# Kernel optimization log

Hardware: AMD Instinct MI355X
Metric: run time of the kernel (lower is better)

Reference implementation:

```python
import jax, jax.numpy as jnp
import numpy as np

N, E, D_IN, D_OUT, MAX_DEG = 50000, 800000, 128, 128, 64
ALPHA = 0.5


def _linear_params(key, fan_in, fan_out):
    s = 1.0 / np.sqrt(fan_in)
    kw, kb = jax.random.split(key)
    W = jax.random.uniform(kw, (fan_out, fan_in), jnp.float32, -s, s)
    b = jax.random.uniform(kb, (fan_out,), jnp.float32, -s, s)
    return W, b


def setup_inputs() -> dict:
    key = jax.random.key(0)
    ks = jax.random.split(key, 16)
    x = jax.random.normal(ks[0], (N, D_IN), jnp.float32)
    edge_index = jax.random.randint(ks[1], (2, E), 0, N, dtype=jnp.int64)
    in_degree = jax.random.randint(ks[2], (N,), 0, MAX_DEG, dtype=jnp.int64)
    out_degree = jax.random.randint(ks[3], (N,), 0, MAX_DEG, dtype=jnp.int64)
    out_deg_mask = jax.random.uniform(ks[4], (N,), jnp.float32)
    out_deg_mask_bias = jax.random.uniform(ks[5], (N,), jnp.float32)
    in_deg_mask = jax.random.uniform(ks[6], (N,), jnp.float32)
    in_deg_mask_bias = jax.random.uniform(ks[7], (N,), jnp.float32)
    W_src, b_src = _linear_params(ks[8], D_IN, D_OUT)
    W_dst, b_dst = _linear_params(ks[9], D_IN, D_OUT)
    W_out_f, b_out_f = _linear_params(ks[10], D_IN, 1)
    W_in_f, b_in_f = _linear_params(ks[11], D_IN, 1)
    W_fc, b_fc = _linear_params(ks[12], D_IN, D_OUT)
    # degree embedding tables, padding_idx=0 -> row 0 zeroed
    in_deg_table = (jax.random.normal(ks[13], (MAX_DEG, D_IN), jnp.float32)).at[0].set(0.0)
    out_deg_table = (jax.random.normal(ks[14], (MAX_DEG, D_IN), jnp.float32)).at[0].set(0.0)
    return {
        "x": x, "edge_index": edge_index,
        "in_degree": in_degree, "out_degree": out_degree,
        "out_deg_mask": out_deg_mask, "out_deg_mask_bias": out_deg_mask_bias,
        "in_deg_mask": in_deg_mask, "in_deg_mask_bias": in_deg_mask_bias,
        "W_src": W_src, "b_src": b_src, "W_dst": W_dst, "b_dst": b_dst,
        "W_out_f": W_out_f, "b_out_f": b_out_f, "W_in_f": W_in_f, "b_in_f": b_in_f,
        "W_fc": W_fc, "b_fc": b_fc,
        "in_deg_table": in_deg_table, "out_deg_table": out_deg_table,
    }


def reference(x, edge_index, in_degree, out_degree,
              out_deg_mask, out_deg_mask_bias, in_deg_mask, in_deg_mask_bias,
              W_src, b_src, W_dst, b_dst,
              W_out_f, b_out_f, W_in_f, b_in_f,
              W_fc, b_fc, in_deg_table, out_deg_table):
    n = x.shape[0]
    row, col = edge_index[0], edge_index[1]
    ones = jnp.ones(row.shape[0], x.dtype)
    # directed norm D_out^{-1/2} A D_in^{-1/2}; transpose reuses the same edge weights
    out_deg = jax.ops.segment_sum(ones, row, num_segments=n)
    in_deg = jax.ops.segment_sum(ones, col, num_segments=n)
    o_inv = jnp.where(out_deg > 0, jax.lax.rsqrt(jnp.maximum(out_deg, 1e-12)), 0.0)
    i_inv = jnp.where(in_deg > 0, jax.lax.rsqrt(jnp.maximum(in_deg, 1e-12)), 0.0)
    w = o_inv[row] * i_inv[col]  # [E]
    # adj_norm @ x and adj_t_norm @ x (SpMM via gather + segment_sum)
    out_nei = jax.ops.segment_sum(w[:, None] * x[col], row, num_segments=n)  # [N,D]
    in_nei = jax.ops.segment_sum(w[:, None] * x[row], col, num_segments=n)   # [N,D]
    # degree-gated filter
    c_out = (out_nei - x + out_deg_table[out_degree]) @ W_out_f.T + b_out_f  # [N,1]
    c_in = (in_nei - x + in_deg_table[in_degree]) @ W_in_f.T + b_in_f        # [N,1]
    C = jax.nn.softmax(jnp.concatenate([c_out, c_in], axis=1), axis=1)        # tau_softmax, tau=1
    C_out = C[:, 0:1] * out_deg_mask[:, None] + out_deg_mask_bias[:, None]
    C_in = C[:, 1:2] * in_deg_mask[:, None] + in_deg_mask_bias[:, None]
    out = (C_out * (out_nei @ W_src.T + b_src)
           + C_in * (in_nei @ W_dst.T + b_dst)
           + ALPHA * (x @ W_fc.T + b_fc))
    return out, C_in, C_out
```

## Files before the change

kernel.cpp:

```cpp
#include <hip/hip_runtime.h>

#define NN 50000
#define EE 800000
#define DD 128
#define CAP 48
#define MT 64
#define XSL 6250
#define PB 128

typedef short short8_t __attribute__((ext_vector_type(8)));
typedef float f32x4 __attribute__((ext_vector_type(4)));

__device__ __forceinline__ unsigned short f2bf(float f) {
    union { float f; unsigned int i; } v; v.f = f;
    unsigned int x = v.i;
    x += 0x7FFFu + ((x >> 16) & 1u);
    return (unsigned short)(x >> 16);
}
__device__ __forceinline__ unsigned int pack2(float a, float b) {
    return (unsigned int)f2bf(a) | ((unsigned int)f2bf(b) << 16);
}
__device__ __forceinline__ float2 bf2x2(unsigned int u) {
    union { unsigned int i; float f; } lo, hi;
    lo.i = u << 16;
    hi.i = u & 0xFFFF0000u;
    return make_float2(lo.f, hi.f);
}

__device__ __forceinline__ void acc8(float4& a, float4& b, uint4 u, float w) {
    float2 p0 = bf2x2(u.x), p1 = bf2x2(u.y), p2 = bf2x2(u.z), p3 = bf2x2(u.w);
    a.x += w * p0.x; a.y += w * p0.y; a.z += w * p1.x; a.w += w * p1.y;
    b.x += w * p2.x; b.y += w * p2.y; b.z += w * p3.x; b.w += w * p3.y;
}

__global__ void k_conv(const float* __restrict__ x,
                       const float* __restrict__ W_src,
                       const float* __restrict__ W_dst,
                       const float* __restrict__ W_fc,
                       unsigned short* __restrict__ xb,
                       unsigned short* __restrict__ wbf) {
    int t = blockIdx.x * 256 + threadIdx.x;
    int base = t * 4;
    if (base < NN * DD) {
        float4 v = *(const float4*)(x + base);
        uint2 p; p.x = pack2(v.x, v.y); p.y = pack2(v.z, v.w);
        *(uint2*)(xb + base) = p;
    } else {
        int b2 = base - NN * DD;
        if (b2 < 3 * 16384) {
            int src = b2 >> 14;
            int off = b2 & 16383;
            const float* W = (src == 0) ? W_src : (src == 1) ? W_dst : W_fc;
            float sc = (src == 2) ? 0.5f : 1.0f;
            float4 v = *(const float4*)(W + off);
            uint2 p; p.x = pack2(v.x * sc, v.y * sc); p.y = pack2(v.z * sc, v.w * sc);
            *(uint2*)(wbf + b2) = p;
        }
    }
}

__global__ void __launch_bounds__(256) k_place(
    const int* __restrict__ ei, int* __restrict__ cnt,
    unsigned short* __restrict__ bkt_row, unsigned short* __restrict__ bkt_col) {
    int xcd = blockIdx.x & 7;
    int b   = blockIdx.x >> 3;
    int lo = xcd * XSL, hi = lo + XSL;
    for (int e = b * 256 + threadIdx.x; e < EE; e += PB * 256) {
        int r = ei[e];
        int c = ei[EE + e];
        if (r >= lo && r < hi) {
            int po = atomicAdd(&cnt[r], 1);
            if (po < CAP) bkt_row[(size_t)r * CAP + po] = (unsigned short)c;
        }
        if (c >= lo && c < hi) {
            int pi = atomicAdd(&cnt[NN + c], 1);
            if (pi < CAP) bkt_col[(size_t)c * CAP + pi] = (unsigned short)r;
        }
    }
}

__global__ void __launch_bounds__(256) k_prep(
    const int* __restrict__ cnt, const float4* __restrict__ x4,
    float* __restrict__ invb, float* __restrict__ w2, uint2* __restrict__ xs2)
{
    int t = blockIdx.x * 256 + threadIdx.x;
    if (t < 2 * NN) {
        int d = cnt[t];
        invb[t] = (d > 0) ? (1.0f / sqrtf((float)d)) : 0.0f;
    }
    if (t < NN) {
        int dd = cnt[t];
        int di = cnt[NN + t];
        float o = (dd > 0) ? (1.0f / sqrtf((float)dd)) : 0.0f;
        w2[t] = (di > 0) ? o * sqrtf((float)di) : o;
    }
    if (t < NN * 32) {
        int node = t >> 5;
        int di = cnt[NN + node];
        float s = (di > 0) ? (1.0f / sqrtf((float)di)) : 1.0f;
        float4 v = x4[t];
        uint2 p; p.x = pack2(v.x * s, v.y * s); p.y = pack2(v.z * s, v.w * s);
        xs2[t] = p;
    }
}

__global__ void __launch_bounds__(256) k_gather(
    const uint4* __restrict__ xs4, const float4* __restrict__ x4,
    const unsigned short* __restrict__ bkt_row, const unsigned short* __restrict__ bkt_col,
    const int* __restrict__ cnt,
    const float* __restrict__ o_inv, const float* __restrict__ i_inv,
    const float* __restrict__ w2,
    const int* __restrict__ in_degree, const int* __restrict__ out_degree,
    const float* __restrict__ odm, const float* __restrict__ odmb,
    const float* __restrict__ idm, const float* __restrict__ idmb,
    const float4* __restrict__ W_out_f4, const float* __restrict__ b_out_f,
    const float4* __restrict__ W_in_f4, const float* __restrict__ b_in_f,
    const float4* __restrict__ in_tab4, const float4* __restrict__ out_tab4,
    uint2* __restrict__ onb2, uint2* __restrict__ inb2,
    float* __restrict__ scbuf,
    float* __restrict__ outCin, float* __restrict__ outCout)
{
    __shared__ float4 sred[2][4][2][16][2];
    __shared__ float sg[2][2];
    __shared__ float sC[2][2];
    int half = threadIdx.x >> 7;
    int n = blockIdx.x * 2 + half;
    int t = threadIdx.x & 127;
    int g = t >> 5;
    int l = t & 31;
    int dir = g >> 1;
    int gd  = g & 1;
    int sub = l >> 4;
    int li  = l & 15;
    int shamt = gd << 4;

    const unsigned short* bp = ((dir == 0) ? bkt_row : bkt_col) + (size_t)n * CAP;
    int deg = cnt[dir * NN + n]; deg = (deg > CAP) ? CAP : deg;

    unsigned int bw = (l < 24) ? *(const unsigned int*)(bp + 2 * l) : 0u;

    float w_l = 0.0f;
    if (dir == 1) {
        unsigned int pr = __shfl(bw, l >> 1, 32);
        int il = (pr >> ((l & 1) << 4)) & 0xffff;
        if (l < deg) w_l = w2[il];
    }

    float4 ac0 = make_float4(0.f, 0.f, 0.f, 0.f);
    float4 ac1 = make_float4(0.f, 0.f, 0.f, 0.f);

    if (dir == 0 || deg <= 32) {
        int j = gd;
        for (; j + 14 < deg; j += 16) {
            int s0 = j + 2 * sub, s1 = s0 + 4, s2 = s0 + 8, s3 = s0 + 12;
            int i0 = (__shfl(bw, s0 >> 1, 32) >> shamt) & 0xffff;
            int i1 = (__shfl(bw, s1 >> 1, 32) >> shamt) & 0xffff;
            int i2 = (__shfl(bw, s2 >> 1, 32) >> shamt) & 0xffff;
            int i3 = (__shfl(bw, s3 >> 1, 32) >> shamt) & 0xffff;
            uint4 u0 = xs4[(size_t)i0 * 16 + li];
            uint4 u1 = xs4[(size_t)i1 * 16 + li];
            uint4 u2 = xs4[(size_t)i2 * 16 + li];
            uint4 u3 = xs4[(size_t)i3 * 16 + li];
            float w0 = 1.f, w1 = 1.f, w2v = 1.f, w3 = 1.f;
            if (dir) {
                w0  = __shfl(w_l, s0, 32);
                w1  = __shfl(w_l, s1, 32);
                w2v = __shfl(w_l, s2, 32);
                w3  = __shfl(w_l, s3, 32);
            }
            acc8(ac0, ac1, u0, w0);
            acc8(ac0, ac1, u1, w1);
            acc8(ac0, ac1, u2, w2v);
            acc8(ac0, ac1, u3, w3);
        }
        for (; j + 6 < deg; j += 8) {
            int s0 = j + 2 * sub, s1 = s0 + 4;
            int i0 = (__shfl(bw, s0 >> 1, 32) >> shamt) & 0xffff;
            int i1 = (__shfl(bw, s1 >> 1, 32) >> shamt) & 0xffff;
            uint4 u0 = xs4[(size_t)i0 * 16 + li];
            uint4 u1 = xs4[(size_t)i1 * 16 + li];
            float w0 = 1.f, w1 = 1.f;
            if (dir) {
                w0 = __shfl(w_l, s0, 32);
                w1 = __shfl(w_l, s1, 32);
            }
            acc8(ac0, ac1, u0, w0);
            acc8(ac0, ac1, u1, w1);
        }
        for (; j < deg; j += 4) {
            int s0 = j + 2 * sub;
            int sc = (s0 < deg) ? s0 : gd;
            int i0 = (__shfl(bw, sc >> 1, 32) >> shamt) & 0xffff;
            float w0 = 1.f;
            if (dir) w0 = __shfl(w_l, sc, 32);
            if (s0 < deg) {
                uint4 u0 = xs4[(size_t)i0 * 16 + li];
                acc8(ac0, ac1, u0, w0);
            }
        }
    } else {
        for (int j = gd; j < deg; j += 4) {
            int s0 = j + 2 * sub;
            int sc = (s0 < deg) ? s0 : gd;
            int i0 = (__shfl(bw, sc >> 1, 32) >> shamt) & 0xffff;
            if (s0 < deg) {
                float w0 = w2[i0];
                uint4 u0 = xs4[(size_t)i0 * 16 + li];
                acc8(ac0, ac1, u0, w0);
            }
        }
    }

    sred[half][g][sub][li][0] = ac0;
    sred[half][g][sub][li][1] = ac1;
    __syncthreads();

    float4 r = make_float4(0.f, 0.f, 0.f, 0.f);
    if (gd == 0) {
        int src = l >> 1, q = l & 1;
        int g0 = dir * 2;
        float4 b0 = sred[half][g0][0][src][q];
        float4 b1 = sred[half][g0][1][src][q];
        float4 b2 = sred[half][g0 + 1][0][src][q];
        float4 b3 = sred[half][g0 + 1][1][src][q];
        float wn = (dir == 0) ? o_inv[n] : i_inv[n];
        r.x = wn * (b0.x + b1.x + b2.x + b3.x);
        r.y = wn * (b0.y + b1.y + b2.y + b3.y);
        r.z = wn * (b0.z + b1.z + b2.z + b3.z);
        r.w = wn * (b0.w + b1.w + b2.w + b3.w);
        float4 xv = x4[(size_t)n * 32 + l];
        float4 tb, wf;
        if (dir == 0) {
            int odg = out_degree[n];
            odg = (odg < 0) ? 0 : (odg > 63 ? 63 : odg);
            tb = out_tab4[(size_t)odg * 32 + l];
            wf = W_out_f4[l];
        } else {
            int idg = in_degree[n];
            idg = (idg < 0) ? 0 : (idg > 63 ? 63 : idg);
            tb = in_tab4[(size_t)idg * 32 + l];
            wf = W_in_f4[l];
        }
        float p = (r.x - xv.x + tb.x) * wf.x + (r.y - xv.y + tb.y) * wf.y
                + (r.z - xv.z + tb.z) * wf.z + (r.w - xv.w + tb.w) * wf.w;
        #pragma unroll
        for (int off = 16; off > 0; off >>= 1) p += __shfl_down(p, off);
        if (l == 0) sg[half][dir] = p;
    }
    __syncthreads();
    if (t == 0) {
        float c_out = sg[half][0] + b_out_f[0];
        float c_in  = sg[half][1] + b_in_f[0];
        float m  = fmaxf(c_out, c_in);
        float eo = expf(c_out - m);
        float e2 = expf(c_in  - m);
        float inv = 1.0f / (eo + e2);
        float Cout = (eo * inv) * odm[n] + odmb[n];
        float Cin  = (e2 * inv) * idm[n] + idmb[n];
        sC[half][0] = Cout; sC[half][1] = Cin;
        scbuf[2 * n]     = Cout;
        scbuf[2 * n + 1] = Cin;
        outCout[n] = Cout;
        outCin[n]  = Cin;
    }
    __syncthreads();
    if (gd == 0) {
        float C = sC[half][dir];
        uint2 pw; pw.x = pack2(C * r.x, C * r.y); pw.y = pack2(C * r.z, C * r.w);
        ((dir == 0) ? onb2 : inb2)[(size_t)n * 32 + l] = pw;
    }
}

__global__ void __launch_bounds__(256) k_gemm(
    const unsigned int* __restrict__ xb32,
    const unsigned int* __restrict__ onb32, const unsigned int* __restrict__ inb32,
    const unsigned short* __restrict__ wbf,
    const float* __restrict__ b_src, const float* __restrict__ b_dst,
    const float* __restrict__ b_fc,
    const float* __restrict__ scbuf,
    float* __restrict__ out)
{
    __shared__ unsigned short sA[MT * 72];
    __shared__ unsigned short sBt[DD * 72];

    int tid = threadIdx.x;
    int wid = tid >> 6;
    int lane = tid & 63;
    int ml = lane & 15;
    int kq = lane >> 4;
    int n0 = blockIdx.x * MT;

    f32x4 accv[8];
    #pragma unroll
    for (int i = 0; i < 8; i++) accv[i] = (f32x4)0.0f;

    const unsigned int* srcs[3] = { onb32, inb32, xb32 };

    for (int kt = 0; kt < 6; kt++) {
        int srcsel = kt >> 1;
        int k0 = (kt & 1) * 64;
        const unsigned int* S = srcs[srcsel];

        #pragma unroll
        for (int r = 0; r < 2; r++) {
            int s = tid + 256 * r;
            int row = s >> 3;
            int cg = s & 7;
            int gn = n0 + row;
            uint4 p = make_uint4(0u, 0u, 0u, 0u);
            if (gn < NN) {
                p = *(const uint4*)(S + (size_t)gn * 64 + (k0 >> 1) + cg * 4);
            }
            *(uint4*)(sA + row * 72 + cg * 8) = p;
        }
        #pragma unroll
        for (int r = 0; r < 4; r++) {
            int s = tid + 256 * r;
            int row = s >> 3;
            int cg = s & 7;
            uint4 w = *(const uint4*)(wbf + srcsel * 16384 + row * DD + k0 + cg * 8);
            *(uint4*)(sBt + row * 72 + cg * 8) = w;
        }
        __syncthreads();

        #pragma unroll
        for (int ks = 0; ks < 64; ks += 32) {
            short8_t a = *(const short8_t*)(sA + (16 * wid + ml) * 72 + ks + kq * 8);
            #pragma unroll
            for (int i = 0; i < 8; i++) {
                short8_t b = *(const short8_t*)(sBt + (16 * i + ml) * 72 + ks + kq * 8);
                accv[i] = __builtin_amdgcn_mfma_f32_16x16x32_bf16(a, b, accv[i], 0, 0, 0);
            }
        }
        __syncthreads();
    }

    int row_base = n0 + 16 * wid + 4 * kq;
    #pragma unroll
    for (int r = 0; r < 4; r++) {
        int row = row_base + r;
        if (row >= NN) continue;
        float Cout = scbuf[2 * row];
        float Cin  = scbuf[2 * row + 1];
        #pragma unroll
        for (int i = 0; i < 8; i++) {
            int col = 16 * i + ml;
            out[(size_t)row * DD + col] =
                accv[i][r] + Cout * b_src[col] + Cin * b_dst[col] + 0.5f * b_fc[col];
        }
    }
}

extern "C" void kernel_launch(void* const* d_in, const int* in_sizes, int n_in,
                              void* d_out, int out_size, void* d_ws, size_t ws_size,
                              hipStream_t stream) {
    const float* x    = (const float*)d_in[0];
    const int* ei     = (const int*)d_in[1];
    const int* in_degree  = (const int*)d_in[2];
    const int* out_degree = (const int*)d_in[3];
    const float* odm  = (const float*)d_in[4];
    const float* odmb = (const float*)d_in[5];
    const float* idm  = (const float*)d_in[6];
    const float* idmb = (const float*)d_in[7];
    const float* W_src = (const float*)d_in[8];
    const float* b_src = (const float*)d_in[9];
    const float* W_dst = (const float*)d_in[10];
    const float* b_dst = (const float*)d_in[11];
    const float* W_out_f = (const float*)d_in[12];
    const float* b_out_f = (const float*)d_in[13];
    const float* W_in_f  = (const float*)d_in[14];
    const float* b_in_f  = (const float*)d_in[15];
    const float* W_fc    = (const float*)d_in[16];
    const float* b_fc    = (const float*)d_in[17];
    const float* in_tab  = (const float*)d_in[18];
    const float* out_tab = (const float*)d_in[19];

    unsigned short* xb  = (unsigned short*)d_ws;
    unsigned short* onb = xb + (size_t)NN * DD;
    unsigned short* inb = onb + (size_t)NN * DD;
    unsigned short* xs  = inb + (size_t)NN * DD;
    float* scbuf = (float*)(xs + (size_t)NN * DD);
    float* invb  = scbuf + 2 * NN;
    float* w2    = invb + 2 * NN;
    unsigned short* wbf = (unsigned short*)(w2 + NN);
    int* cnt     = (int*)(wbf + 3 * 16384);
    unsigned short* bkt_row = (unsigned short*)(cnt + 2 * NN);
    unsigned short* bkt_col = bkt_row + (size_t)NN * CAP;

    hipMemsetAsync(cnt, 0, (size_t)2 * NN * sizeof(int), stream);

    int conv_quads = (NN * DD + 3 * 16384) / 4;
    k_conv<<<(conv_quads + 255) / 256, 256, 0, stream>>>(x, W_src, W_dst, W_fc, xb, wbf);
    k_place<<<8 * PB, 256, 0, stream>>>(ei, cnt, bkt_row, bkt_col);
    k_prep<<<(NN * 32 + 255) / 256, 256, 0, stream>>>(cnt, (const float4*)x,
                                                      invb, w2, (uint2*)xs);

    float* o_inv = invb;
    float* i_inv = invb + NN;
    float* out_p  = (float*)d_out;
    float* cin_p  = out_p + (size_t)NN * DD;
    float* cout_p = cin_p + NN;

    k_gather<<<NN / 2, 256, 0, stream>>>((const uint4*)xs, (const float4*)x,
                                         bkt_row, bkt_col, cnt,
                                         o_inv, i_inv, w2, in_degree, out_degree,
                                         odm, odmb, idm, idmb,
                                         (const float4*)W_out_f, b_out_f,
                                         (const float4*)W_in_f, b_in_f,
                                         (const float4*)in_tab, (const float4*)out_tab,
                                         (uint2*)onb, (uint2*)inb,
                                         scbuf, cin_p, cout_p);

    k_gemm<<<(NN + MT - 1) / MT, 256, 0, stream>>>(
        (const unsigned int*)xb, (const unsigned int*)onb, (const unsigned int*)inb,
        wbf, b_src, b_dst, b_fc, scbuf, out_p);
}
```

Baseline: 285.5 us.

## Fuse bucket placement with bf16 conversion and use packed f32 accumulation

Measured after the change: 275.1 us. -3.6%, faster.

```diff
diff --git a/kernel.cpp b/kernel.cpp
--- a/kernel.cpp
+++ b/kernel.cpp
@@ -7,9 +7,11 @@
 #define MT 64
 #define XSL 6250
 #define PB 128
+#define PCB (8 * PB)
 
 typedef short short8_t __attribute__((ext_vector_type(8)));
 typedef float f32x4 __attribute__((ext_vector_type(4)));
+typedef float f32x2 __attribute__((ext_vector_type(2)));
 
 __device__ __forceinline__ unsigned short f2bf(float f) {
     union { float f; unsigned int i; } v; v.f = f;
@@ -26,55 +28,71 @@
     hi.i = u & 0xFFFF0000u;
     return make_float2(lo.f, hi.f);
 }
-
-__device__ __forceinline__ void acc8(float4& a, float4& b, uint4 u, float w) {
-    float2 p0 = bf2x2(u.x), p1 = bf2x2(u.y), p2 = bf2x2(u.z), p3 = bf2x2(u.w);
-    a.x += w * p0.x; a.y += w * p0.y; a.z += w * p1.x; a.w += w * p1.y;
-    b.x += w * p2.x; b.y += w * p2.y; b.z += w * p3.x; b.w += w * p3.y;
-}
-
-__global__ void k_conv(const float* __restrict__ x,
-                       const float* __restrict__ W_src,
-                       const float* __restrict__ W_dst,
-                       const float* __restrict__ W_fc,
-                       unsigned short* __restrict__ xb,
-                       unsigned short* __restrict__ wbf) {
-    int t = blockIdx.x * 256 + threadIdx.x;
-    int base = t * 4;
-    if (base < NN * DD) {
-        float4 v = *(const float4*)(x + base);
-        uint2 p; p.x = pack2(v.x, v.y); p.y = pack2(v.z, v.w);
-        *(uint2*)(xb + base) = p;
+__device__ __forceinline__ f32x2 bfup(unsigned int u) {
+    union { unsigned int i; float f; } lo, hi;
+    lo.i = u << 16;
+    hi.i = u & 0xFFFF0000u;
+    f32x2 r; r.x = lo.f; r.y = hi.f;
+    return r;
+}
+__device__ __forceinline__ void pkadd(f32x2& a, f32x2 b) {
+    asm("v_pk_add_f32 %0, %1, %0" : "+v"(a) : "v"(b));
+}
+__device__ __forceinline__ void pkfma(f32x2& a, f32x2 b, f32x2 w) {
+    asm("v_pk_fma_f32 %0, %1, %2, %0" : "+v"(a) : "v"(b), "v"(w));
+}
+__device__ __forceinline__ void accnw(f32x2* ac, uint4 u) {
+    pkadd(ac[0], bfup(u.x)); pkadd(ac[1], bfup(u.y));
+    pkadd(ac[2], bfup(u.z)); pkadd(ac[3], bfup(u.w));
+}
+__device__ __forceinline__ void accw(f32x2* ac, uint4 u, float w) {
+    f32x2 wp; wp.x = w; wp.y = w;
+    pkfma(ac[0], bfup(u.x), wp); pkfma(ac[1], bfup(u.y), wp);
+    pkfma(ac[2], bfup(u.z), wp); pkfma(ac[3], bfup(u.w), wp);
+}
+
+__global__ void __launch_bounds__(256) k_pc(
+    const int* __restrict__ ei, int* __restrict__ cnt,
+    unsigned short* __restrict__ bkt_row, unsigned short* __restrict__ bkt_col,
+    const float* __restrict__ x,
+    const float* __restrict__ W_src, const float* __restrict__ W_dst,
+    const float* __restrict__ W_fc,
+    unsigned short* __restrict__ xb, unsigned short* __restrict__ wbf)
+{
+    if (blockIdx.x < PCB) {
+        int xcd = blockIdx.x & 7;
+        int b   = blockIdx.x >> 3;
+        int lo = xcd * XSL, hi = lo + XSL;
+        for (int e = b * 256 + threadIdx.x; e < EE; e += PB * 256) {
+            int r = ei[e];
+            int c = ei[EE + e];
+            if (r >= lo && r < hi) {
+                int po = atomicAdd(&cnt[r], 1);
+                if (po < CAP) bkt_row[(size_t)r * CAP + po] = (unsigned short)c;
+            }
+            if (c >= lo && c < hi) {
+                int pi = atomicAdd(&cnt[NN + c], 1);
+                if (pi < CAP) bkt_col[(size_t)c * CAP + pi] = (unsigned short)r;
+            }
+        }
     } else {
-        int b2 = base - NN * DD;
-        if (b2 < 3 * 16384) {
-            int src = b2 >> 14;
-            int off = b2 & 16383;
-            const float* W = (src == 0) ? W_src : (src == 1) ? W_dst : W_fc;
-            float sc = (src == 2) ? 0.5f : 1.0f;
-            float4 v = *(const float4*)(W + off);
-            uint2 p; p.x = pack2(v.x * sc, v.y * sc); p.y = pack2(v.z * sc, v.w * sc);
-            *(uint2*)(wbf + b2) = p;
-        }
-    }
-}
-
-__global__ void __launch_bounds__(256) k_place(
-    const int* __restrict__ ei, int* __restrict__ cnt,
-    unsigned short* __restrict__ bkt_row, unsigned short* __restrict__ bkt_col) {
-    int xcd = blockIdx.x & 7;
-    int b   = blockIdx.x >> 3;
-    int lo = xcd * XSL, hi = lo + XSL;
-    for (int e = b * 256 + threadIdx.x; e < EE; e += PB * 256) {
-        int r = ei[e];
-        int c = ei[EE + e];
-        if (r >= lo && r < hi) {
-            int po = atomicAdd(&cnt[r], 1);
-            if (po < CAP) bkt_row[(size_t)r * CAP + po] = (unsigned short)c;
-        }
-        if (c >= lo && c < hi) {
-            int pi = atomicAdd(&cnt[NN + c], 1);
-            if (pi < CAP) bkt_col[(size_t)c * CAP + pi] = (unsigned short)r;
+        int t = (blockIdx.x - PCB) * 256 + threadIdx.x;
+        int base = t * 4;
+        if (base < NN * DD) {
+            float4 v = *(const float4*)(x + base);
+            uint2 p; p.x = pack2(v.x, v.y); p.y = pack2(v.z, v.w);
+            *(uint2*)(xb + base) = p;
+        } else {
+            int b2 = base - NN * DD;
+            if (b2 < 3 * 16384) {
+                int src = b2 >> 14;
+                int off = b2 & 16383;
+                const float* W = (src == 0) ? W_src : (src == 1) ? W_dst : W_fc;
+                float sc = (src == 2) ? 0.5f : 1.0f;
+                float4 v = *(const float4*)(W + off);
+                uint2 p; p.x = pack2(v.x * sc, v.y * sc); p.y = pack2(v.z * sc, v.w * sc);
+                *(uint2*)(wbf + b2) = p;
+            }
         }
     }
 }
@@ -120,7 +138,7 @@
     float* __restrict__ scbuf,
     float* __restrict__ outCin, float* __restrict__ outCout)
 {
-    __shared__ float4 sred[2][4][2][16][2];
+    __shared__ float4 sred[2][4][2][16][3];
     __shared__ float sg[2][2];
     __shared__ float sC[2][2];
     int half = threadIdx.x >> 7;
@@ -146,10 +164,41 @@
         if (l < deg) w_l = w2[il];
     }
 
-    float4 ac0 = make_float4(0.f, 0.f, 0.f, 0.f);
-    float4 ac1 = make_float4(0.f, 0.f, 0.f, 0.f);
-
-    if (dir == 0 || deg <= 32) {
+    f32x2 ac[4];
+    ac[0] = (f32x2)0.0f; ac[1] = (f32x2)0.0f; ac[2] = (f32x2)0.0f; ac[3] = (f32x2)0.0f;
+
+    if (dir == 0) {
+        int j = gd;
+        for (; j + 14 < deg; j += 16) {
+            int s0 = j + 2 * sub;
+            int i0 = (__shfl(bw, s0 >> 1, 32) >> shamt) & 0xffff;
+            int i1 = (__shfl(bw, (s0 + 4) >> 1, 32) >> shamt) & 0xffff;
+            int i2 = (__shfl(bw, (s0 + 8) >> 1, 32) >> shamt) & 0xffff;
+            int i3 = (__shfl(bw, (s0 + 12) >> 1, 32) >> shamt) & 0xffff;
+            uint4 u0 = xs4[(size_t)i0 * 16 + li];
+            uint4 u1 = xs4[(size_t)i1 * 16 + li];
+            uint4 u2 = xs4[(size_t)i2 * 16 + li];
+            uint4 u3 = xs4[(size_t)i3 * 16 + li];
+            accnw(ac, u0); accnw(ac, u1); accnw(ac, u2); accnw(ac, u3);
+        }
+        for (; j + 6 < deg; j += 8) {
+            int s0 = j + 2 * sub;
+            int i0 = (__shfl(bw, s0 >> 1, 32) >> shamt) & 0xffff;
+            int i1 = (__shfl(bw, (s0 + 4) >> 1, 32) >> shamt) & 0xffff;
+            uint4 u0 = xs4[(size_t)i0 * 16 + li];
+            uint4 u1 = xs4[(size_t)i1 * 16 + li];
+            accnw(ac, u0); accnw(ac, u1);
+        }
+        for (; j < deg; j += 4) {
+            int s0 = j + 2 * sub;
+            int sc = (s0 < deg) ? s0 : gd;
+            int i0 = (__shfl(bw, sc >> 1, 32) >> shamt) & 0xffff;
+            if (s0 < deg) {
+                uint4 u0 = xs4[(size_t)i0 * 16 + li];
+                accnw(ac, u0);
+            }
+        }
+    } else if (deg <= 32) {
         int j = gd;
         for (; j + 14 < deg; j += 16) {
             int s0 = j + 2 * sub, s1 = s0 + 4, s2 = s0 + 8, s3 = s0 + 12;
@@ -161,17 +210,11 @@
             uint4 u1 = xs4[(size_t)i1 * 16 + li];
             uint4 u2 = xs4[(size_t)i2 * 16 + li];
             uint4 u3 = xs4[(size_t)i3 * 16 + li];
-            float w0 = 1.f, w1 = 1.f, w2v = 1.f, w3 = 1.f;
-            if (dir) {
-                w0  = __shfl(w_l, s0, 32);
-                w1  = __shfl(w_l, s1, 32);
-                w2v = __shfl(w_l, s2, 32);
-                w3  = __shfl(w_l, s3, 32);
-            }
-            acc8(ac0, ac1, u0, w0);
-            acc8(ac0, ac1, u1, w1);
-            acc8(ac0, ac1, u2, w2v);
-            acc8(ac0, ac1, u3, w3);
+            float w0 = __shfl(w_l, s0, 32);
+            float w1 = __shfl(w_l, s1, 32);
+            float w2v = __shfl(w_l, s2, 32);
+            float w3 = __shfl(w_l, s3, 32);
+            accw(ac, u0, w0); accw(ac, u1, w1); accw(ac, u2, w2v); accw(ac, u3, w3);
         }
         for (; j + 6 < deg; j += 8) {
             int s0 = j + 2 * sub, s1 = s0 + 4;
@@ -179,23 +222,18 @@
             int i1 = (__shfl(bw, s1 >> 1, 32) >> shamt) & 0xffff;
             uint4 u0 = xs4[(size_t)i0 * 16 + li];
             uint4 u1 = xs4[(size_t)i1 * 16 + li];
-            float w0 = 1.f, w1 = 1.f;
-            if (dir) {
-                w0 = __shfl(w_l, s0, 32);
-                w1 = __shfl(w_l, s1, 32);
-            }
-            acc8(ac0, ac1, u0, w0);
-            acc8(ac0, ac1, u1, w1);
+            float w0 = __shfl(w_l, s0, 32);
+            float w1 = __shfl(w_l, s1, 32);
+            accw(ac, u0, w0); accw(ac, u1, w1);
         }
         for (; j < deg; j += 4) {
             int s0 = j + 2 * sub;
             int sc = (s0 < deg) ? s0 : gd;
             int i0 = (__shfl(bw, sc >> 1, 32) >> shamt) & 0xffff;
-            float w0 = 1.f;
-            if (dir) w0 = __shfl(w_l, sc, 32);
+            float w0 = __shfl(w_l, sc, 32);
             if (s0 < deg) {
                 uint4 u0 = xs4[(size_t)i0 * 16 + li];
-                acc8(ac0, ac1, u0, w0);
+                accw(ac, u0, w0);
             }
         }
     } else {
@@ -206,13 +244,13 @@
             if (s0 < deg) {
                 float w0 = w2[i0];
                 uint4 u0 = xs4[(size_t)i0 * 16 + li];
-                acc8(ac0, ac1, u0, w0);
-            }
-        }
-    }
-
-    sred[half][g][sub][li][0] = ac0;
-    sred[half][g][sub][li][1] = ac1;
+                accw(ac, u0, w0);
+            }
+        }
+    }
+
+    sred[half][g][sub][li][0] = make_float4(ac[0].x, ac[0].y, ac[1].x, ac[1].y);
+    sred[half][g][sub][li][1] = make_float4(ac[2].x, ac[2].y, ac[3].x, ac[3].y);
     __syncthreads();
 
     float4 r = make_float4(0.f, 0.f, 0.f, 0.f);
@@ -390,8 +428,9 @@
     hipMemsetAsync(cnt, 0, (size_t)2 * NN * sizeof(int), stream);
 
     int conv_quads = (NN * DD + 3 * 16384) / 4;
-    k_conv<<<(conv_quads + 255) / 256, 256, 0, stream>>>(x, W_src, W_dst, W_fc, xb, wbf);
-    k_place<<<8 * PB, 256, 0, stream>>>(ei, cnt, bkt_row, bkt_col);
+    int conv_blocks = (conv_quads + 255) / 256;
+    k_pc<<<PCB + conv_blocks, 256, 0, stream>>>(ei, cnt, bkt_row, bkt_col,
+                                                x, W_src, W_dst, W_fc, xb, wbf);
     k_prep<<<(NN * 32 + 255) / 256, 256, 0, stream>>>(cnt, (const float4*)x,
                                                       invb, w2, (uint2*)xs);
 
```
